# Performance work log

Hardware: AMD Instinct MI355X
Metric: run time of the kernel (lower is better)

The kernel has to match this reference:

```python
import jax, jax.numpy as jnp
import numpy as np

B, N, C, O, K = 8, 1024, 64, 64, 3  # batch, nodes, in_c, out_c, Cheb order
EPS = 1e-12


def setup_inputs() -> dict:
    key = jax.random.key(0)
    ks = jax.random.split(key, 10)
    X_real = jax.random.normal(ks[0], (B, N, C), dtype=jnp.float32)
    X_imag = jax.random.normal(ks[1], (B, N, C), dtype=jnp.float32)
    L_real = jax.random.normal(ks[2], (B, K + 1, N, N), dtype=jnp.float32)
    L_imag = jax.random.normal(ks[3], (B, K + 1, N, N), dtype=jnp.float32)
    # Chebyshev weights: uniform(-stdv, stdv) then normalized to unit complex magnitude (as in __init__)
    stdv = 1.0 / np.sqrt(O)
    w_real = jax.random.uniform(ks[4], (K + 1, C, O), minval=-stdv, maxval=stdv, dtype=jnp.float32)
    w_imag = jax.random.uniform(ks[5], (K + 1, C, O), minval=-stdv, maxval=stdv, dtype=jnp.float32)
    mag = jnp.sqrt(w_real ** 2 + w_imag ** 2)
    w_real = w_real / mag
    w_imag = w_imag / mag
    # complex attention linear: maps 2*C -> 1
    a_stdv = 1.0 / np.sqrt(2 * C)
    attn_w_real = jax.random.uniform(ks[6], (2 * C,), minval=-a_stdv, maxval=a_stdv, dtype=jnp.float32)
    attn_w_imag = jax.random.uniform(ks[7], (2 * C,), minval=-a_stdv, maxval=a_stdv, dtype=jnp.float32)
    attn_b_real = jnp.zeros((1,), dtype=jnp.float32)
    attn_b_imag = jnp.zeros((1,), dtype=jnp.float32)
    # complex PReLU slopes (PyTorch PReLU default init 0.25)
    prelu_a_real = jnp.full((1,), 0.25, dtype=jnp.float32)
    prelu_a_imag = jnp.full((1,), 0.25, dtype=jnp.float32)
    return dict(X_real=X_real, X_imag=X_imag, L_real=L_real, L_imag=L_imag,
                w_real=w_real, w_imag=w_imag,
                attn_w_real=attn_w_real, attn_w_imag=attn_w_imag,
                attn_b_real=attn_b_real, attn_b_imag=attn_b_imag,
                prelu_a_real=prelu_a_real, prelu_a_imag=prelu_a_imag)


def reference(X_real, X_imag, L_real, L_imag, w_real, w_imag,
              attn_w_real, attn_w_imag, attn_b_real, attn_b_imag,
              prelu_a_real, prelu_a_imag):
    c = X_real.shape[-1]
    # --- attention scores: CVLinear on concat(x_i, x_j) decomposes into per-node terms ---
    Wr_i, Wr_j = attn_w_real[:c], attn_w_real[c:]
    Wi_i, Wi_j = attn_w_imag[:c], attn_w_imag[c:]
    sR_i = X_real @ Wr_i - X_imag @ Wi_i  # [B,N]
    sI_i = X_real @ Wi_i + X_imag @ Wr_i
    sR_j = X_real @ Wr_j - X_imag @ Wi_j
    sI_j = X_real @ Wi_j + X_imag @ Wr_j
    scores_r = sR_i[:, :, None] + sR_j[:, None, :] + attn_b_real  # [B,N,N]
    scores_i = sI_i[:, :, None] + sI_j[:, None, :] + attn_b_imag
    # --- complex PReLU (applied to real/imag separately) ---
    pr = jnp.where(scores_r >= 0, scores_r, prelu_a_real * scores_r)
    pi = jnp.where(scores_i >= 0, scores_i, prelu_a_imag * scores_i)
    # --- phase softmax over dim=1: softmax of magnitude, phase preserved ---
    mag = jnp.sqrt(pr ** 2 + pi ** 2)
    sm = jax.nn.softmax(mag, axis=1)
    scale = sm / (mag + EPS)
    ar = scale * pr  # [B,N,N] complex attention (real part)
    ai = scale * pi
    # --- modulate complex Laplacian stack [B,K+1,N,N] ---
    Lr = L_real * ar[:, None] - L_imag * ai[:, None]
    Li = L_real * ai[:, None] + L_imag * ar[:, None]
    # einsum 'bijk,bqjp->bijp' with q-size 1 == rowsum over k, then scale X per node j
    rowR = Lr.sum(-1)  # [B,K+1,N]
    rowI = Li.sum(-1)
    # complex (L-rowsum * X) @ W, summed over the K+1 terms (torch.sum dim=2 of stack)
    real = (jnp.einsum('bmj,bjc,mco->bjo', rowR, X_real, w_real)
            - jnp.einsum('bmj,bjc,mco->bjo', rowI, X_imag, w_imag))
    imag = (jnp.einsum('bmj,bjc,mco->bjo', rowI, X_real, w_real)
            + jnp.einsum('bmj,bjc,mco->bjo', rowR, X_imag, w_imag))
    return real, imag
```

## Files before the change

kernel.cpp:

```cpp
#include <hip/hip_runtime.h>

#define EPS_Q 1e-12f

__device__ __forceinline__ float wave_reduce_sum(float v) {
#pragma unroll
    for (int m = 32; m > 0; m >>= 1) v += __shfl_xor(v, m, 64);
    return v;
}

__global__ __launch_bounds__(256)
void k_scores(const float* __restrict__ Xr, const float* __restrict__ Xi,
              const float* __restrict__ awr, const float* __restrict__ awi,
              float* __restrict__ sRi, float* __restrict__ sIi,
              float4* __restrict__ aux) {
    const int lane = threadIdx.x & 63;
    const int row  = (blockIdx.x << 2) + (threadIdx.x >> 6);
    const float xr = Xr[row * 64 + lane];
    const float xi = Xi[row * 64 + lane];
    const float wri = awr[lane], wrj = awr[64 + lane];
    const float wii = awi[lane], wij = awi[64 + lane];
    float v0 = xr * wri - xi * wii;
    float v1 = xr * wii + xi * wri;
    float v2 = xr * wrj - xi * wij;
    float v3 = xr * wij + xi * wrj;
#pragma unroll
    for (int m = 32; m > 0; m >>= 1) {
        v0 += __shfl_xor(v0, m, 64);
        v1 += __shfl_xor(v1, m, 64);
        v2 += __shfl_xor(v2, m, 64);
        v3 += __shfl_xor(v3, m, 64);
    }
    if (lane == 0) {
        sRi[row] = v0;
        sIi[row] = v1;
        aux[row].x = v2;
        aux[row].y = v3;
    }
}

__global__ __launch_bounds__(256)
void k_softmax(const float* __restrict__ sRi, const float* __restrict__ sIi,
               float4* __restrict__ aux,
               const float* __restrict__ abr, const float* __restrict__ abi,
               const float* __restrict__ par_, const float* __restrict__ pai_) {
    const int lane = threadIdx.x & 63;
    const int row  = (blockIdx.x << 2) + (threadIdx.x >> 6);
    const int b    = row >> 10;
    const float br = abr[0], bi = abi[0], par = par_[0], pai = pai_[0];
    const float sRj = aux[row].x, sIj = aux[row].y;
    const float* pR = sRi + (b << 10);
    const float* pI = sIi + (b << 10);
    float mags[16];
    float mx = -3.4e38f;
#pragma unroll
    for (int t = 0; t < 16; ++t) {
        const int i = (t << 6) + lane;
        float sr = pR[i] + sRj + br;
        float si = pI[i] + sIj + bi;
        float pr = sr >= 0.f ? sr : par * sr;
        float pi = si >= 0.f ? si : pai * si;
        float mg = sqrtf(pr * pr + pi * pi);
        mags[t] = mg;
        mx = fmaxf(mx, mg);
    }
#pragma unroll
    for (int m = 32; m > 0; m >>= 1) mx = fmaxf(mx, __shfl_xor(mx, m, 64));
    float s = 0.f;
#pragma unroll
    for (int t = 0; t < 16; ++t) s += __expf(mags[t] - mx);
    s = wave_reduce_sum(s);
    if (lane == 0) {
        aux[row].z = mx;
        aux[row].w = 1.f / s;
    }
}

__global__ __launch_bounds__(256)
void k_rowreduce(const float* __restrict__ Lr, const float* __restrict__ Li,
                 const float* __restrict__ sRi, const float* __restrict__ sIi,
                 const float4* __restrict__ aux,
                 const float* __restrict__ abr, const float* __restrict__ abi,
                 const float* __restrict__ par_, const float* __restrict__ pai_,
                 float* __restrict__ rowR, float* __restrict__ rowI) {
    const int lane = threadIdx.x & 63;
    const int row  = (blockIdx.x << 2) + (threadIdx.x >> 6);
    const int b = row >> 10;
    const int i = row & 1023;
    const float br = abr[0], bi = abi[0], par = par_[0], pai = pai_[0];
    const float sri = sRi[row], sii = sIi[row];
    const float4* auxb = aux + (b << 10);
    const size_t base = ((size_t)((b * 4) * 1024 + i)) * 1024;
    const float4* LR = (const float4*)(Lr + base);
    const float4* LI = (const float4*)(Li + base);
    const int kstr = (1024 * 1024) / 4;
    float aR[4] = {0.f, 0.f, 0.f, 0.f};
    float aI[4] = {0.f, 0.f, 0.f, 0.f};
#pragma unroll
    for (int t = 0; t < 4; ++t) {
        const int j4 = (t << 6) + lane;
        float arj[4], aij[4];
#pragma unroll
        for (int u = 0; u < 4; ++u) {
            const float4 ax = auxb[(j4 << 2) + u];
            float sr = sri + ax.x + br;
            float si = sii + ax.y + bi;
            float pr = sr >= 0.f ? sr : par * sr;
            float pi = si >= 0.f ? si : pai * si;
            float mg = sqrtf(pr * pr + pi * pi);
            float sc = __expf(mg - ax.z) * ax.w / (mg + EPS_Q);
            arj[u] = sc * pr;
            aij[u] = sc * pi;
        }
#pragma unroll
        for (int k = 0; k < 4; ++k) {
            const float4 lr = LR[k * kstr + j4];
            const float4 li = LI[k * kstr + j4];
            aR[k] += lr.x * arj[0] - li.x * aij[0];
            aR[k] += lr.y * arj[1] - li.y * aij[1];
            aR[k] += lr.z * arj[2] - li.z * aij[2];
            aR[k] += lr.w * arj[3] - li.w * aij[3];
            aI[k] += lr.x * aij[0] + li.x * arj[0];
            aI[k] += lr.y * aij[1] + li.y * arj[1];
            aI[k] += lr.z * aij[2] + li.z * arj[2];
            aI[k] += lr.w * aij[3] + li.w * arj[3];
        }
    }
#pragma unroll
    for (int m = 32; m > 0; m >>= 1) {
#pragma unroll
        for (int k = 0; k < 4; ++k) {
            aR[k] += __shfl_xor(aR[k], m, 64);
            aI[k] += __shfl_xor(aI[k], m, 64);
        }
    }
    if (lane == 0) {
#pragma unroll
        for (int k = 0; k < 4; ++k) {
            rowR[((b << 2) + k) * 1024 + i] = aR[k];
            rowI[((b << 2) + k) * 1024 + i] = aI[k];
        }
    }
}

__global__ __launch_bounds__(256)
void k_output(const float* __restrict__ Xr, const float* __restrict__ Xi,
              const float* __restrict__ wr, const float* __restrict__ wi,
              const float* __restrict__ rowR, const float* __restrict__ rowI,
              float* __restrict__ out) {
    __shared__ float lxr[16][64];
    __shared__ float lxi[16][64];
    const int tid = threadIdx.x;
    const int rb  = blockIdx.x << 4;
    {
        const float4* s0 = (const float4*)(Xr + (size_t)rb * 64);
        const float4* s1 = (const float4*)(Xi + (size_t)rb * 64);
        ((float4*)&lxr[0][0])[tid] = s0[tid];
        ((float4*)&lxi[0][0])[tid] = s1[tid];
    }
    __syncthreads();
    const int wave = tid >> 6, lane = tid & 63;
    const int r0 = wave << 2;
    float u[4][4], v[4][4];
#pragma unroll
    for (int r = 0; r < 4; ++r)
#pragma unroll
        for (int m = 0; m < 4; ++m) { u[r][m] = 0.f; v[r][m] = 0.f; }
    for (int c = 0; c < 64; ++c) {
        float wrv[4], wiv[4];
#pragma unroll
        for (int m = 0; m < 4; ++m) {
            wrv[m] = wr[((m << 6) + c) * 64 + lane];
            wiv[m] = wi[((m << 6) + c) * 64 + lane];
        }
#pragma unroll
        for (int r = 0; r < 4; ++r) {
            const float xr = lxr[r0 + r][c];
            const float xi = lxi[r0 + r][c];
#pragma unroll
            for (int m = 0; m < 4; ++m) {
                u[r][m] += xr * wrv[m];
                v[r][m] += xi * wiv[m];
            }
        }
    }
#pragma unroll
    for (int r = 0; r < 4; ++r) {
        const int row = rb + r0 + r;
        const int b = row >> 10, j = row & 1023;
        float re = 0.f, im = 0.f;
#pragma unroll
        for (int m = 0; m < 4; ++m) {
            const float rr = rowR[(b << 12) + (m << 10) + j];
            const float ri = rowI[(b << 12) + (m << 10) + j];
            re += rr * u[r][m] - ri * v[r][m];
            im += ri * u[r][m] + rr * v[r][m];
        }
        out[(size_t)row * 64 + lane] = re;
        out[524288 + (size_t)row * 64 + lane] = im;
    }
}

extern "C" void kernel_launch(void* const* d_in, const int* in_sizes, int n_in,
                              void* d_out, int out_size, void* d_ws, size_t ws_size,
                              hipStream_t stream) {
    const float* Xr  = (const float*)d_in[0];
    const float* Xi  = (const float*)d_in[1];
    const float* Lr  = (const float*)d_in[2];
    const float* Li  = (const float*)d_in[3];
    const float* wr  = (const float*)d_in[4];
    const float* wi  = (const float*)d_in[5];
    const float* awr = (const float*)d_in[6];
    const float* awi = (const float*)d_in[7];
    const float* abr = (const float*)d_in[8];
    const float* abi = (const float*)d_in[9];
    const float* par = (const float*)d_in[10];
    const float* pai = (const float*)d_in[11];
    float* out = (float*)d_out;

    float*  ws   = (float*)d_ws;
    float*  sRi  = ws;
    float*  sIi  = ws + 8192;
    float4* aux  = (float4*)(ws + 16384);
    float*  rowR = ws + 49152;
    float*  rowI = ws + 81920;

    k_scores  <<<dim3(2048), dim3(256), 0, stream>>>(Xr, Xi, awr, awi, sRi, sIi, aux);
    k_softmax <<<dim3(2048), dim3(256), 0, stream>>>(sRi, sIi, aux, abr, abi, par, pai);
    k_rowreduce<<<dim3(2048), dim3(256), 0, stream>>>(Lr, Li, sRi, sIi, aux,
                                                      abr, abi, par, pai, rowR, rowI);
    k_output  <<<dim3(512),  dim3(256), 0, stream>>>(Xr, Xi, wr, wi, rowR, rowI, out);
}
```

Measured before the change: 354.5 us.

## Assign one row per block, one Chebyshev order per wave, and precompute attention in LDS

```diff
diff --git a/kernel.cpp b/kernel.cpp
--- a/kernel.cpp
+++ b/kernel.cpp
@@ -82,63 +82,62 @@
                  const float* __restrict__ abr, const float* __restrict__ abi,
                  const float* __restrict__ par_, const float* __restrict__ pai_,
                  float* __restrict__ rowR, float* __restrict__ rowI) {
-    const int lane = threadIdx.x & 63;
-    const int row  = (blockIdx.x << 2) + (threadIdx.x >> 6);
+    __shared__ float lar[1024];
+    __shared__ float lai[1024];
+    const int tid = threadIdx.x;
+    const int row = blockIdx.x;
     const int b = row >> 10;
     const int i = row & 1023;
     const float br = abr[0], bi = abi[0], par = par_[0], pai = pai_[0];
     const float sri = sRi[row], sii = sIi[row];
     const float4* auxb = aux + (b << 10);
-    const size_t base = ((size_t)((b * 4) * 1024 + i)) * 1024;
+
+#pragma unroll
+    for (int t = 0; t < 4; ++t) {
+        const int j = (t << 8) + tid;
+        const float4 ax = auxb[j];
+        float sr = sri + ax.x + br;
+        float si = sii + ax.y + bi;
+        float pr = sr >= 0.f ? sr : par * sr;
+        float pi = si >= 0.f ? si : pai * si;
+        float mg = sqrtf(pr * pr + pi * pi);
+        float sc = __expf(mg - ax.z) * ax.w / (mg + EPS_Q);
+        lar[j] = sc * pr;
+        lai[j] = sc * pi;
+    }
+    __syncthreads();
+
+    const int wave = tid >> 6, lane = tid & 63;
+    const size_t base = ((size_t)((b * 4 + wave) * 1024 + i)) * 1024;
     const float4* LR = (const float4*)(Lr + base);
     const float4* LI = (const float4*)(Li + base);
-    const int kstr = (1024 * 1024) / 4;
-    float aR[4] = {0.f, 0.f, 0.f, 0.f};
-    float aI[4] = {0.f, 0.f, 0.f, 0.f};
+    const float4* AR = (const float4*)lar;
+    const float4* AI = (const float4*)lai;
+    float aR = 0.f, aI = 0.f;
 #pragma unroll
     for (int t = 0; t < 4; ++t) {
         const int j4 = (t << 6) + lane;
-        float arj[4], aij[4];
-#pragma unroll
-        for (int u = 0; u < 4; ++u) {
-            const float4 ax = auxb[(j4 << 2) + u];
-            float sr = sri + ax.x + br;
-            float si = sii + ax.y + bi;
-            float pr = sr >= 0.f ? sr : par * sr;
-            float pi = si >= 0.f ? si : pai * si;
-            float mg = sqrtf(pr * pr + pi * pi);
-            float sc = __expf(mg - ax.z) * ax.w / (mg + EPS_Q);
-            arj[u] = sc * pr;
-            aij[u] = sc * pi;
-        }
-#pragma unroll
-        for (int k = 0; k < 4; ++k) {
-            const float4 lr = LR[k * kstr + j4];
-            const float4 li = LI[k * kstr + j4];
-            aR[k] += lr.x * arj[0] - li.x * aij[0];
-            aR[k] += lr.y * arj[1] - li.y * aij[1];
-            aR[k] += lr.z * arj[2] - li.z * aij[2];
-            aR[k] += lr.w * arj[3] - li.w * aij[3];
-            aI[k] += lr.x * aij[0] + li.x * arj[0];
-            aI[k] += lr.y * aij[1] + li.y * arj[1];
-            aI[k] += lr.z * aij[2] + li.z * arj[2];
-            aI[k] += lr.w * aij[3] + li.w * arj[3];
-        }
+        const float4 lr = LR[j4];
+        const float4 li = LI[j4];
+        const float4 ar = AR[j4];
+        const float4 ai = AI[j4];
+        aR += lr.x * ar.x - li.x * ai.x;
+        aR += lr.y * ar.y - li.y * ai.y;
+        aR += lr.z * ar.z - li.z * ai.z;
+        aR += lr.w * ar.w - li.w * ai.w;
+        aI += lr.x * ai.x + li.x * ar.x;
+        aI += lr.y * ai.y + li.y * ar.y;
+        aI += lr.z * ai.z + li.z * ar.z;
+        aI += lr.w * ai.w + li.w * ar.w;
     }
 #pragma unroll
     for (int m = 32; m > 0; m >>= 1) {
-#pragma unroll
-        for (int k = 0; k < 4; ++k) {
-            aR[k] += __shfl_xor(aR[k], m, 64);
-            aI[k] += __shfl_xor(aI[k], m, 64);
-        }
+        aR += __shfl_xor(aR, m, 64);
+        aI += __shfl_xor(aI, m, 64);
     }
     if (lane == 0) {
-#pragma unroll
-        for (int k = 0; k < 4; ++k) {
-            rowR[((b << 2) + k) * 1024 + i] = aR[k];
-            rowI[((b << 2) + k) * 1024 + i] = aI[k];
-        }
+        rowR[((b << 2) + wave) * 1024 + i] = aR;
+        rowI[((b << 2) + wave) * 1024 + i] = aI;
     }
 }
 
@@ -226,7 +225,7 @@
 
     k_scores  <<<dim3(2048), dim3(256), 0, stream>>>(Xr, Xi, awr, awi, sRi, sIi, aux);
     k_softmax <<<dim3(2048), dim3(256), 0, stream>>>(sRi, sIi, aux, abr, abi, par, pai);
-    k_rowreduce<<<dim3(2048), dim3(256), 0, stream>>>(Lr, Li, sRi, sIi, aux,
+    k_rowreduce<<<dim3(8192), dim3(256), 0, stream>>>(Lr, Li, sRi, sIi, aux,
                                                       abr, abi, par, pai, rowR, rowI);
     k_output  <<<dim3(512),  dim3(256), 0, stream>>>(Xr, Xi, wr, wi, rowR, rowI, out);
 }
```

New measurement: 341.9 us. 1.04x faster.
